# Kernel tuning notes

Measured on AMD Instinct MI355X. Metric: run time of the kernel, lower is better.

## Reference

```python
import jax, jax.numpy as jnp
import numpy as np

N = 100000
E = 800000
D_IN = 128
D_HID = 128
D_EMB = 128
D_OUT = 2


def setup_inputs() -> dict:
    key = jax.random.key(0)
    ks = jax.random.split(key, 16)
    x = jax.random.normal(ks[0], (N, D_IN), dtype=jnp.float32)
    edge_index = jax.random.randint(ks[1], (2, E), 0, N, dtype=jnp.int64)

    def lin(k, d_out, d_in, scale):
        return jax.random.normal(k, (d_out, d_in), dtype=jnp.float32) * scale

    s1 = 1.0 / np.sqrt(D_IN)
    s2 = 1.0 / np.sqrt(D_HID)
    s3 = 1.0 / np.sqrt(D_EMB)
    return {
        "x": x,
        "edge_index": edge_index,
        # layer 1: in -> hidden  (lin_l has bias, lin_r no bias, as in PyG SAGEConv)
        "Wl1": lin(ks[2], D_HID, D_IN, s1), "bl1": jnp.zeros((D_HID,), jnp.float32),
        "Wr1": lin(ks[3], D_HID, D_IN, s1),
        # layer 2: hidden -> hidden
        "Wl2": lin(ks[4], D_HID, D_HID, s2), "bl2": jnp.zeros((D_HID,), jnp.float32),
        "Wr2": lin(ks[5], D_HID, D_HID, s2),
        # layer 3: hidden -> embedding
        "Wl3": lin(ks[6], D_EMB, D_HID, s2), "bl3": jnp.zeros((D_EMB,), jnp.float32),
        "Wr3": lin(ks[7], D_EMB, D_HID, s2),
        # output head: embedding -> output (bias)
        "Wo": lin(ks[8], D_OUT, D_EMB, s3), "bo": jnp.zeros((D_OUT,), jnp.float32),
    }


def _sage_conv(x, src, dst, Wl, bl, Wr):
    # mean-aggregate neighbor (source) features onto destination nodes
    msg = x[src]                                             # [E, d]
    agg = jax.ops.segment_sum(msg, dst, num_segments=N)      # [N, d]
    deg = jax.ops.segment_sum(jnp.ones((src.shape[0],), x.dtype), dst, num_segments=N)
    agg = agg / jnp.maximum(deg, 1.0)[:, None]
    # out = lin_l(agg) + lin_r(x)
    return agg @ Wl.T + bl + x @ Wr.T


def reference(x, edge_index, Wl1, bl1, Wr1, Wl2, bl2, Wr2, Wl3, bl3, Wr3, Wo, bo):
    src, dst = edge_index[0], edge_index[1]
    h = jax.nn.relu(_sage_conv(x, src, dst, Wl1, bl1, Wr1))   # dropout is identity in eval
    h = jax.nn.relu(_sage_conv(h, src, dst, Wl2, bl2, Wr2))
    h = _sage_conv(h, src, dst, Wl3, bl3, Wr3)                # no relu on last conv
    return h @ Wo.T + bo                                      # [N, D_OUT]
```

## Files before the change

### kernel.cpp

```cpp
#include <hip/hip_runtime.h>
#include <stdint.h>

typedef unsigned int u32;
typedef unsigned short u16;
typedef __bf16 bf16x8 __attribute__((ext_vector_type(8)));
typedef float floatx16 __attribute__((ext_vector_type(16)));
typedef u32 u32x4 __attribute__((ext_vector_type(4)));
typedef float floatx4 __attribute__((ext_vector_type(4)));

__device__ __forceinline__ u16 f2b(float f) {
    u32 u = __builtin_bit_cast(u32, f);
    u32 r = u + 0x7FFFu + ((u >> 16) & 1u);
    return (u16)(r >> 16);
}
__device__ __forceinline__ float lo2f(u32 u) { return __builtin_bit_cast(float, u << 16); }
__device__ __forceinline__ float hi2f(u32 u) { return __builtin_bit_cast(float, u & 0xFFFF0000u); }


__device__ __forceinline__ void self_detect(const int* ei, const u32* xw, int& is64, int& isbf) {
    int lane = threadIdx.x & 63;
    int v = ei ? ei[2 * lane + 1] : 0;
    unsigned long long b1 = __ballot(v == 0);
    u32 w = xw ? xw[lane] : 0;
    u32 e = (w >> 7) & 0xFF;
    int plaus = (e == 0) || (e >= 90 && e <= 140);
    unsigned long long b2 = __ballot(plaus);
    is64 = (b1 == ~0ULL) ? 1 : 0;
    isbf = (b2 == ~0ULL) ? 1 : 0;
}

__device__ __forceinline__ int load_id(const int* __restrict__ ei, int is64, size_t pos, int N) {
    int v = is64 ? ei[2 * pos] : ei[pos];
    unsigned u = (unsigned)v;
    if (u >= (unsigned)N) u = 0;
    return (int)u;
}

__device__ __forceinline__ float load_f(const void* __restrict__ p, int isbf, size_t i) {
    if (isbf) {
        u16 s = ((const u16*)p)[i];
        return __builtin_bit_cast(float, ((u32)s) << 16);
    }
    return ((const float*)p)[i];
}


__global__ void pre_kernel(const void* __restrict__ xraw, int N, int cb,
                           u32* __restrict__ xb,
                           const void* Wl1, const void* Wr1, const void* Wl2, const void* Wr2,
                           const void* Wl3, const void* Wr3, const void* b1, const void* b2,
                           const void* b3, const void* Wo, const void* bo,
                           u16* __restrict__ Wcp, float* __restrict__ smalls) {
    int is64, isbf;
    self_detect(nullptr, (const u32*)xraw, is64, isbf);
    int blk = blockIdx.x;
    if (blk < cb) {
        int i = blk * 256 + threadIdx.x;
        int count4 = N * 16;
        if (i >= count4) return;
        if (isbf) {
            ((u32x4*)xb)[i] = ((const u32x4*)xraw)[i];
        } else {
            const floatx4* f4 = (const floatx4*)xraw;
            floatx4 f0 = f4[2 * i], f1 = f4[2 * i + 1];
            u32x4 o;
            o.x = (u32)f2b(f0.x) | ((u32)f2b(f0.y) << 16);
            o.y = (u32)f2b(f0.z) | ((u32)f2b(f0.w) << 16);
            o.z = (u32)f2b(f1.x) | ((u32)f2b(f1.y) << 16);
            o.w = (u32)f2b(f1.z) | ((u32)f2b(f1.w) << 16);
            ((u32x4*)xb)[i] = o;
        }
    } else {
        int wblk = blk - cb;
        if (wblk < 48) {
            int l = wblk >> 4;
            const void* Wl = (l == 0) ? Wl1 : (l == 1) ? Wl2 : Wl3;
            const void* Wr = (l == 0) ? Wr1 : (l == 1) ? Wr2 : Wr3;
            u16* Wout = Wcp + (size_t)l * 32768;
            int t = (wblk & 15) * 256 + threadIdx.x;
            int lane = t & 63;
            int jt = (t >> 6) & 3;
            int s = t >> 8;
            int n = lane & 31;
            int q = lane >> 5;
            int j = jt * 32 + n;
#pragma unroll
            for (int jj = 0; jj < 8; ++jj) {
                int k = s * 16 + q * 8 + jj;
                float v = (k < 128) ? load_f(Wl, isbf, (size_t)j * 128 + k)
                                    : load_f(Wr, isbf, (size_t)j * 128 + (k - 128));
                Wout[t * 8 + jj] = f2b(v);
            }
        } else {
            for (int t = threadIdx.x; t < 642; t += 256) {
                float v;
                if (t < 128) v = load_f(b1, isbf, t);
                else if (t < 256) v = load_f(b2, isbf, t - 128);
                else if (t < 384) v = load_f(b3, isbf, t - 256);
                else if (t < 640) v = load_f(Wo, isbf, t - 384);
                else v = load_f(bo, isbf, t - 640);
                smalls[t] = v;
            }
        }
    }
}


#define CH 4096
#define CAPB 3072

__global__ void bucket_scatter_kernel(const int* __restrict__ ei, int E, int N,
                                      int* __restrict__ gcur, u32* __restrict__ csrbkt) {
    __shared__ int lhist[1024], loff[1024], lcur[1024], gofs[1024], wsum[16];
    __shared__ u32 ebuf[CH];
    __shared__ u16 ebkt[CH];
    int t = threadIdx.x;
    int is64, isbf;
    self_detect(ei, nullptr, is64, isbf);
    int cbase = blockIdx.x * CH;
    int cn = E - cbase;
    if (cn > CH) cn = CH;
    lhist[t] = 0;
    __syncthreads();
    int mysrc[4], myb[4], mydl[4];
#pragma unroll
    for (int k = 0; k < 4; ++k) {
        int i = t + k * 1024;
        myb[k] = -1;
        if (i < cn) {
            int e = cbase + i;
            int s = load_id(ei, is64, (size_t)e, N);
            int d = load_id(ei, is64, (size_t)E + e, N);
            mysrc[k] = s;
            mydl[k] = d & 255;
            myb[k] = d >> 8;
            atomicAdd(&lhist[myb[k]], 1);
        }
    }
    __syncthreads();
    int lane = t & 63, wid = t >> 6;
    int v = lhist[t];
    int inc = v;
#pragma unroll
    for (int off = 1; off < 64; off <<= 1) {
        int o = __shfl_up(inc, off);
        if (lane >= off) inc += o;
    }
    if (lane == 63) wsum[wid] = inc;
    __syncthreads();
    int wpre = 0;
    for (int w = 0; w < wid; ++w) wpre += wsum[w];
    int excl = wpre + inc - v;
    loff[t] = excl;
    lcur[t] = excl;
    if (v > 0) gofs[t] = atomicAdd(&gcur[t], v);
    __syncthreads();
#pragma unroll
    for (int k = 0; k < 4; ++k) {
        if (myb[k] >= 0) {
            int pos = atomicAdd(&lcur[myb[k]], 1);
            ebuf[pos] = (u32)mysrc[k] | ((u32)mydl[k] << 24);
            ebkt[pos] = (u16)myb[k];
        }
    }
    __syncthreads();
#pragma unroll
    for (int k = 0; k < 4; ++k) {
        int i = t + k * 1024;
        if (i < cn) {
            int bb = ebkt[i];
            int local = gofs[bb] + (i - loff[bb]);
            if (local < CAPB) csrbkt[(size_t)bb * CAPB + local] = ebuf[i];
        }
    }
}

__global__ void csr_build_kernel(const u32* __restrict__ csrbkt, const int* __restrict__ gcur,
                                 int N, int* __restrict__ gtot,
                                 int* __restrict__ offs, int* __restrict__ cnt,
                                 int* __restrict__ csr) {
    __shared__ int lh[256], lcur[256], wsum[4];
    __shared__ int sbase;
    __shared__ u32 sbuf[CAPB];
    int t = threadIdx.x;
    int b = blockIdx.x;
    int cb = gcur[b];
    if (cb > CAPB) cb = CAPB;
    const u32* bsrc = csrbkt + (size_t)b * CAPB;
    int d0 = b << 8;
    lh[t] = 0;
    __syncthreads();
    for (int i = t; i < cb; i += 256) atomicAdd(&lh[bsrc[i] >> 24], 1);
    __syncthreads();
    int lane = t & 63, wid = t >> 6;
    int v = lh[t];
    int inc = v;
#pragma unroll
    for (int off = 1; off < 64; off <<= 1) {
        int o = __shfl_up(inc, off);
        if (lane >= off) inc += o;
    }
    if (lane == 63) wsum[wid] = inc;
    __syncthreads();
    int wpre = 0;
    for (int w = 0; w < wid; ++w) wpre += wsum[w];
    int excl = wpre + inc - v;
    lcur[t] = excl;
    if (t == 0) sbase = atomicAdd(gtot, cb);
    __syncthreads();
    int base = sbase;
    int d = d0 + t;
    if (d < N) {
        offs[d] = base + excl;
        cnt[d] = v;
    }
    for (int i = t; i < cb; i += 256) {
        u32 e = bsrc[i];
        int pos = atomicAdd(&lcur[e >> 24], 1);
        sbuf[pos] = e & 0xFFFFFFu;
    }
    __syncthreads();
    for (int i = t; i < cb; i += 256) csr[base + i] = (int)sbuf[i];
}


__global__ void agg_kernel(const u32* __restrict__ F2, const int* __restrict__ offs,
                           const int* __restrict__ cnt, const int* __restrict__ csr,
                           u32* __restrict__ Aout, int N) {
    int gw = (blockIdx.x * 256 + threadIdx.x) >> 6;
    int lane = threadIdx.x & 63;
    int nd0 = gw * 4;
    if (nd0 >= N) return;
    int nd1 = nd0 + 4 < N ? nd0 + 4 : N;
    for (int nd = nd0; nd < nd1; ++nd) {
        int start = offs[nd];
        int num = cnt[nd];
        float a0 = 0.f, a1 = 0.f;
        int i = 0;
        for (; i + 8 <= num; i += 8) {
            int s0 = csr[start + i + 0], s1 = csr[start + i + 1];
            int s2 = csr[start + i + 2], s3 = csr[start + i + 3];
            int s4 = csr[start + i + 4], s5 = csr[start + i + 5];
            int s6 = csr[start + i + 6], s7 = csr[start + i + 7];
            u32 u0 = F2[(size_t)s0 * 64 + lane];
            u32 u1 = F2[(size_t)s1 * 64 + lane];
            u32 u2 = F2[(size_t)s2 * 64 + lane];
            u32 u3 = F2[(size_t)s3 * 64 + lane];
            u32 u4 = F2[(size_t)s4 * 64 + lane];
            u32 u5 = F2[(size_t)s5 * 64 + lane];
            u32 u6 = F2[(size_t)s6 * 64 + lane];
            u32 u7 = F2[(size_t)s7 * 64 + lane];
            a0 += lo2f(u0) + lo2f(u1) + lo2f(u2) + lo2f(u3) +
                  lo2f(u4) + lo2f(u5) + lo2f(u6) + lo2f(u7);
            a1 += hi2f(u0) + hi2f(u1) + hi2f(u2) + hi2f(u3) +
                  hi2f(u4) + hi2f(u5) + hi2f(u6) + hi2f(u7);
        }
        for (; i + 4 <= num; i += 4) {
            int s0 = csr[start + i + 0], s1 = csr[start + i + 1];
            int s2 = csr[start + i + 2], s3 = csr[start + i + 3];
            u32 u0 = F2[(size_t)s0 * 64 + lane];
            u32 u1 = F2[(size_t)s1 * 64 + lane];
            u32 u2 = F2[(size_t)s2 * 64 + lane];
            u32 u3 = F2[(size_t)s3 * 64 + lane];
            a0 += lo2f(u0) + lo2f(u1) + lo2f(u2) + lo2f(u3);
            a1 += hi2f(u0) + hi2f(u1) + hi2f(u2) + hi2f(u3);
        }
        for (; i < num; ++i) {
            u32 u = F2[(size_t)csr[start + i] * 64 + lane];
            a0 += lo2f(u);
            a1 += hi2f(u);
        }
        float sc = 1.0f / (float)(num > 1 ? num : 1);
        a0 *= sc;
        a1 *= sc;
        Aout[(size_t)nd * 64 + lane] = (u32)f2b(a0) | ((u32)f2b(a1) << 16);
    }
}


__global__ void gemm_kernel(const u32* __restrict__ aggb, u32* Fio,
                            const u16* __restrict__ Wcp, const float* __restrict__ biasf,
                            int N, int relu, const float* __restrict__ headw,
                            const u32* __restrict__ xw, void* __restrict__ outp) {
    int tid = threadIdx.x;
    int w = tid >> 6;
    int lane = tid & 63;
    int nbase = blockIdx.x * 128;
    int n = lane & 31;
    int q = lane >> 5;
    int rowl = w * 32 + n;
    int node = nbase + rowl;
    int nodeC = (node < N) ? node : (N - 1);
    const u32* aRow = aggb + (size_t)nodeC * 64 + q * 4;
    const u32* fRow = Fio + (size_t)nodeC * 64 + q * 4;

    floatx16 acc0 = 0.0f, acc1 = 0.0f, acc2 = 0.0f, acc3 = 0.0f;

#pragma unroll
    for (int s = 0; s < 16; ++s) {
        const u32* ap = (s < 8) ? (aRow + (size_t)s * 8) : (fRow + (size_t)(s - 8) * 8);
        bf16x8 a = *reinterpret_cast<const bf16x8*>(ap);
        const u16* bp = Wcp + (size_t)((s * 4) * 64 + lane) * 8;
        bf16x8 b0 = *reinterpret_cast<const bf16x8*>(bp);
        bf16x8 b1 = *reinterpret_cast<const bf16x8*>(bp + 64 * 8);
        bf16x8 b2 = *reinterpret_cast<const bf16x8*>(bp + 2 * 64 * 8);
        bf16x8 b3 = *reinterpret_cast<const bf16x8*>(bp + 3 * 64 * 8);
        acc0 = __builtin_amdgcn_mfma_f32_32x32x16_bf16(a, b0, acc0, 0, 0, 0);
        acc1 = __builtin_amdgcn_mfma_f32_32x32x16_bf16(a, b1, acc1, 0, 0, 0);
        acc2 = __builtin_amdgcn_mfma_f32_32x32x16_bf16(a, b2, acc2, 0, 0, 0);
        acc3 = __builtin_amdgcn_mfma_f32_32x32x16_bf16(a, b3, acc3, 0, 0, 0);
    }

    int mbase = nbase + w * 32;
    floatx16 accs[4] = {acc0, acc1, acc2, acc3};

    if (outp == nullptr) {
#pragma unroll
        for (int jt = 0; jt < 4; ++jt) {
            int j0 = jt * 32 + n;
            float bf = biasf[j0];
#pragma unroll
            for (int r = 0; r < 16; ++r) {
                int row = (r & 3) + 8 * (r >> 2) + 4 * q;
                int nodeS = mbase + row;
                if (nodeS < N) {
                    float v = accs[jt][r] + bf;
                    if (relu) v = fmaxf(v, 0.0f);
                    u16* dst16 = (u16*)&Fio[(size_t)nodeS * 64];
                    dst16[j0] = f2b(v);
                }
            }
        }
    } else {
        int is64, isbf;
        self_detect(nullptr, xw, is64, isbf);
#pragma unroll
        for (int r = 0; r < 16; ++r) {
            float p0 = 0.f, p1 = 0.f;
#pragma unroll
            for (int jt = 0; jt < 4; ++jt) {
                int j = jt * 32 + n;
                float v = accs[jt][r] + biasf[j];
                p0 += v * headw[j];
                p1 += v * headw[128 + j];
            }
#pragma unroll
            for (int off = 16; off > 0; off >>= 1) {
                p0 += __shfl_xor(p0, off);
                p1 += __shfl_xor(p1, off);
            }
            if (n == 0) {
                int row = (r & 3) + 8 * (r >> 2) + 4 * q;
                int nodeS = mbase + row;
                if (nodeS < N) {
                    float o0 = p0 + headw[256];
                    float o1 = p1 + headw[257];
                    if (isbf)
                        ((u32*)outp)[nodeS] = (u32)f2b(o0) | ((u32)f2b(o1) << 16);
                    else
                        ((float2*)outp)[nodeS] = make_float2(o0, o1);
                }
            }
        }
    }
}

extern "C" void kernel_launch(void* const* d_in, const int* in_sizes, int n_in,
                              void* d_out, int out_size, void* d_ws, size_t ws_size,
                              hipStream_t stream) {
    const int N = in_sizes[0] / 128;
    const int E = in_sizes[1] / 2;

    const void* x = d_in[0];
    const int* ei = (const int*)d_in[1];
    const void* Wl[3] = {d_in[2], d_in[5], d_in[8]};
    const void* bl[3] = {d_in[3], d_in[6], d_in[9]};
    const void* Wr[3] = {d_in[4], d_in[7], d_in[10]};
    const void* Wo = d_in[11];
    const void* bo = d_in[12];

    char* p = (char*)d_ws;
    auto alloc = [&](size_t bytes) -> char* {
        char* r = p;
        p += (bytes + 255) & ~(size_t)255;
        return r;
    };
    int* offs = (int*)alloc((size_t)N * 4);
    int* cnt = (int*)alloc((size_t)N * 4);
    float* smalls = (float*)alloc(642 * 4);
    int* gcur = (int*)alloc(1025 * 4);
    int* csr = (int*)alloc((size_t)E * 4);
    u16* Wcp = (u16*)alloc((size_t)3 * 4096 * 8 * 2);
    u32* xb = (u32*)alloc((size_t)N * 64 * 4);
    u32* aggb = (u32*)alloc((size_t)N * 64 * 4);
    u32* csrbkt = aggb;
    int* gtot = gcur + 1024;
    (void)ws_size;

    const int NB = (N + 255) / 256;
    const int cb = (N * 16 + 255) / 256;
    const int sb = (E + CH - 1) / CH;
    const int gb = (N + 127) / 128;
    const int ab = ((N + 3) / 4 + 3) / 4;

    hipMemsetAsync(gcur, 0, 1025 * 4, stream);
    pre_kernel<<<cb + 49, 256, 0, stream>>>(x, N, cb, xb,
                                            Wl[0], Wr[0], Wl[1], Wr[1], Wl[2], Wr[2],
                                            bl[0], bl[1], bl[2], Wo, bo, Wcp, smalls);
    bucket_scatter_kernel<<<sb, 1024, 0, stream>>>(ei, E, N, gcur, csrbkt);
    csr_build_kernel<<<NB, 256, 0, stream>>>(csrbkt, gcur, N, gtot, offs, cnt, csr);

    agg_kernel<<<ab, 256, 0, stream>>>(xb, offs, cnt, csr, aggb, N);
    gemm_kernel<<<gb, 256, 0, stream>>>(aggb, xb, Wcp, smalls, N, 1, nullptr, nullptr, nullptr);
    agg_kernel<<<ab, 256, 0, stream>>>(xb, offs, cnt, csr, aggb, N);
    gemm_kernel<<<gb, 256, 0, stream>>>(aggb, xb, Wcp + 32768, smalls + 128, N, 1, nullptr, nullptr, nullptr);
    agg_kernel<<<ab, 256, 0, stream>>>(xb, offs, cnt, csr, aggb, N);
    gemm_kernel<<<gb, 256, 0, stream>>>(aggb, xb, Wcp + 65536, smalls + 256, N, 0,
                                        smalls + 384, (const u32*)x, d_out);
}
```

Baseline: 341.3 us.

## Split GEMM output columns across waves and fold memset into pre kernel

The GEMM kernel now gives each block 32 nodes, and each of its four waves computes one 32-column slice with a single accumulator instead of four. This cuts register pressure and raises the block count fourfold, at the cost of every wave reloading the same A rows. The output-head reduction now combines per-wave partials through shared memory. The separate hipMemsetAsync for gcur is dropped and its zeroing moves into an extra block of pre_kernel, saving one launch.

After: 361.6 us. +5.9%, slower.

```diff
diff --git a/kernel.cpp b/kernel.cpp
--- a/kernel.cpp
+++ b/kernel.cpp
@@ -46,7 +46,7 @@
 
 
 __global__ void pre_kernel(const void* __restrict__ xraw, int N, int cb,
-                           u32* __restrict__ xb,
+                           u32* __restrict__ xb, int* __restrict__ gcur,
                            const void* Wl1, const void* Wr1, const void* Wl2, const void* Wr2,
                            const void* Wl3, const void* Wr3, const void* b1, const void* b2,
                            const void* b3, const void* Wo, const void* bo,
@@ -91,7 +91,7 @@
                                     : load_f(Wr, isbf, (size_t)j * 128 + (k - 128));
                 Wout[t * 8 + jj] = f2b(v);
             }
-        } else {
+        } else if (wblk == 48) {
             for (int t = threadIdx.x; t < 642; t += 256) {
                 float v;
                 if (t < 128) v = load_f(b1, isbf, t);
@@ -101,6 +101,8 @@
                 else v = load_f(bo, isbf, t - 640);
                 smalls[t] = v;
             }
+        } else {
+            for (int t = threadIdx.x; t < 1025; t += 256) gcur[t] = 0;
         }
     }
 }
@@ -278,72 +280,55 @@
 }
 
 
-__global__ void gemm_kernel(const u32* __restrict__ aggb, u32* Fio,
-                            const u16* __restrict__ Wcp, const float* __restrict__ biasf,
-                            int N, int relu, const float* __restrict__ headw,
-                            const u32* __restrict__ xw, void* __restrict__ outp) {
+__global__ __launch_bounds__(256) void gemm_kernel(
+    const u32* __restrict__ aggb, u32* Fio, const u16* __restrict__ Wcp,
+    const float* __restrict__ biasf, int N, int relu, const float* __restrict__ headw,
+    const u32* __restrict__ xw, void* __restrict__ outp) {
+    __shared__ float hred[4][32][2];
     int tid = threadIdx.x;
     int w = tid >> 6;
     int lane = tid & 63;
-    int nbase = blockIdx.x * 128;
     int n = lane & 31;
     int q = lane >> 5;
-    int rowl = w * 32 + n;
-    int node = nbase + rowl;
-    int nodeC = (node < N) ? node : (N - 1);
+    int nbase = blockIdx.x * 32;
+    int node = nbase + n;
+    int nodeC = (node < N) ? node : nbase;
     const u32* aRow = aggb + (size_t)nodeC * 64 + q * 4;
     const u32* fRow = Fio + (size_t)nodeC * 64 + q * 4;
 
-    floatx16 acc0 = 0.0f, acc1 = 0.0f, acc2 = 0.0f, acc3 = 0.0f;
-
+    floatx16 acc = 0.0f;
 #pragma unroll
     for (int s = 0; s < 16; ++s) {
         const u32* ap = (s < 8) ? (aRow + (size_t)s * 8) : (fRow + (size_t)(s - 8) * 8);
         bf16x8 a = *reinterpret_cast<const bf16x8*>(ap);
-        const u16* bp = Wcp + (size_t)((s * 4) * 64 + lane) * 8;
-        bf16x8 b0 = *reinterpret_cast<const bf16x8*>(bp);
-        bf16x8 b1 = *reinterpret_cast<const bf16x8*>(bp + 64 * 8);
-        bf16x8 b2 = *reinterpret_cast<const bf16x8*>(bp + 2 * 64 * 8);
-        bf16x8 b3 = *reinterpret_cast<const bf16x8*>(bp + 3 * 64 * 8);
-        acc0 = __builtin_amdgcn_mfma_f32_32x32x16_bf16(a, b0, acc0, 0, 0, 0);
-        acc1 = __builtin_amdgcn_mfma_f32_32x32x16_bf16(a, b1, acc1, 0, 0, 0);
-        acc2 = __builtin_amdgcn_mfma_f32_32x32x16_bf16(a, b2, acc2, 0, 0, 0);
-        acc3 = __builtin_amdgcn_mfma_f32_32x32x16_bf16(a, b3, acc3, 0, 0, 0);
-    }
-
-    int mbase = nbase + w * 32;
-    floatx16 accs[4] = {acc0, acc1, acc2, acc3};
-
+        const u16* bp = Wcp + (size_t)((s * 4 + w) * 64 + lane) * 8;
+        bf16x8 b = *reinterpret_cast<const bf16x8*>(bp);
+        acc = __builtin_amdgcn_mfma_f32_32x32x16_bf16(a, b, acc, 0, 0, 0);
+    }
+    __syncthreads();
+
+    int j0 = w * 32 + n;
     if (outp == nullptr) {
-#pragma unroll
-        for (int jt = 0; jt < 4; ++jt) {
-            int j0 = jt * 32 + n;
-            float bf = biasf[j0];
-#pragma unroll
-            for (int r = 0; r < 16; ++r) {
-                int row = (r & 3) + 8 * (r >> 2) + 4 * q;
-                int nodeS = mbase + row;
-                if (nodeS < N) {
-                    float v = accs[jt][r] + bf;
-                    if (relu) v = fmaxf(v, 0.0f);
-                    u16* dst16 = (u16*)&Fio[(size_t)nodeS * 64];
-                    dst16[j0] = f2b(v);
-                }
+        float bf = biasf[j0];
+#pragma unroll
+        for (int r = 0; r < 16; ++r) {
+            int row = (r & 3) + 8 * (r >> 2) + 4 * q;
+            int nodeS = nbase + row;
+            if (nodeS < N) {
+                float v = acc[r] + bf;
+                if (relu) v = fmaxf(v, 0.0f);
+                ((u16*)&Fio[(size_t)nodeS * 64])[j0] = f2b(v);
             }
         }
     } else {
         int is64, isbf;
         self_detect(nullptr, xw, is64, isbf);
+        float bf = biasf[j0];
+        float w0 = headw[j0], w1 = headw[128 + j0];
 #pragma unroll
         for (int r = 0; r < 16; ++r) {
-            float p0 = 0.f, p1 = 0.f;
-#pragma unroll
-            for (int jt = 0; jt < 4; ++jt) {
-                int j = jt * 32 + n;
-                float v = accs[jt][r] + biasf[j];
-                p0 += v * headw[j];
-                p1 += v * headw[128 + j];
-            }
+            float v = acc[r] + bf;
+            float p0 = v * w0, p1 = v * w1;
 #pragma unroll
             for (int off = 16; off > 0; off >>= 1) {
                 p0 += __shfl_xor(p0, off);
@@ -351,15 +336,23 @@
             }
             if (n == 0) {
                 int row = (r & 3) + 8 * (r >> 2) + 4 * q;
-                int nodeS = mbase + row;
-                if (nodeS < N) {
-                    float o0 = p0 + headw[256];
-                    float o1 = p1 + headw[257];
-                    if (isbf)
-                        ((u32*)outp)[nodeS] = (u32)f2b(o0) | ((u32)f2b(o1) << 16);
-                    else
-                        ((float2*)outp)[nodeS] = make_float2(o0, o1);
-                }
+                hred[w][row][0] = p0;
+                hred[w][row][1] = p1;
+            }
+        }
+        __syncthreads();
+        if (tid < 32) {
+            int row = tid;
+            int nodeS = nbase + row;
+            if (nodeS < N) {
+                float o0 = hred[0][row][0] + hred[1][row][0] + hred[2][row][0] +
+                           hred[3][row][0] + headw[256];
+                float o1 = hred[0][row][1] + hred[1][row][1] + hred[2][row][1] +
+                           hred[3][row][1] + headw[257];
+                if (isbf)
+                    ((u32*)outp)[nodeS] = (u32)f2b(o0) | ((u32)f2b(o1) << 16);
+                else
+                    ((float2*)outp)[nodeS] = make_float2(o0, o1);
             }
         }
     }
@@ -400,11 +393,10 @@
     const int NB = (N + 255) / 256;
     const int cb = (N * 16 + 255) / 256;
     const int sb = (E + CH - 1) / CH;
-    const int gb = (N + 127) / 128;
+    const int gb = (N + 31) / 32;
     const int ab = ((N + 3) / 4 + 3) / 4;
 
-    hipMemsetAsync(gcur, 0, 1025 * 4, stream);
-    pre_kernel<<<cb + 49, 256, 0, stream>>>(x, N, cb, xb,
+    pre_kernel<<<cb + 50, 256, 0, stream>>>(x, N, cb, xb, gcur,
                                             Wl[0], Wr[0], Wl[1], Wr[1], Wl[2], Wr[2],
                                             bl[0], bl[1], bl[2], Wo, bo, Wcp, smalls);
     bucket_scatter_kernel<<<sb, 1024, 0, stream>>>(ei, E, N, gcur, csrbkt);
```
